# Kernel tuning notes

Hardware: AMD Instinct MI355X
Metric: run time of the kernel (lower is better)

Reference implementation:

```python
import jax, jax.numpy as jnp
import numpy as np

B, N, DIM = 4, 16384, 3
HID = 128            # hidden_dim
CDIM = 128           # feature_dim
RESO = 128           # plane_resolution
R2 = RESO * RESO
NBLK = 5             # n_blocks


def setup_inputs() -> dict:
    key = jax.random.key(0)
    ks = jax.random.split(key, 8)
    s = 0.02
    return {
        "points": jax.random.uniform(ks[0], (B, N, DIM), jnp.float32),  # normalized to [0,1)
        "fc_pos_w": jax.random.normal(ks[1], (2 * HID, DIM), jnp.float32) * s,
        "fc_pos_b": jnp.zeros((2 * HID,), jnp.float32),
        "blk_fc0_w": jax.random.normal(ks[2], (NBLK, HID, 2 * HID), jnp.float32) * s,
        "blk_fc0_b": jnp.zeros((NBLK, HID), jnp.float32),
        "blk_fc1_w": jax.random.normal(ks[3], (NBLK, HID, HID), jnp.float32) * s,
        "blk_fc1_b": jnp.zeros((NBLK, HID), jnp.float32),
        "blk_sc_w": jax.random.normal(ks[4], (NBLK, HID, 2 * HID), jnp.float32) * s,
        "fc_c_w": jax.random.normal(ks[5], (CDIM, HID), jnp.float32) * s,
        "fc_c_b": jnp.zeros((CDIM,), jnp.float32),
    }


def _coord2index(coord_xy):
    # coordinate2index: (coord * reso).long(), then x + reso * y
    g = jnp.clip((coord_xy * RESO).astype(jnp.int32), 0, RESO - 1)  # (B, N, 2)
    return g[..., 0] + RESO * g[..., 1]  # (B, N)


def _resblock(x, w0, b0, w1, b1, ws):
    # ResnetBlockFC: shortcut(x) + fc_1(relu(fc_0(relu(x))))
    h = jax.nn.relu(x) @ w0.T + b0          # (B, N, HID)
    dx = jax.nn.relu(h) @ w1.T + b1         # (B, N, HID)
    return x @ ws.T + dx


def _forward(points, fc_pos_w, fc_pos_b, blk_fc0_w, blk_fc0_b,
             blk_fc1_w, blk_fc1_b, blk_sc_w, fc_c_w, fc_c_b):
    idx = _coord2index(points[..., :2])          # (B, N) int32 plane-bin ids
    net = points @ fc_pos_w.T + fc_pos_b          # (B, N, 2*HID)
    net = _resblock(net, blk_fc0_w[0], blk_fc0_b[0], blk_fc1_w[0], blk_fc1_b[0], blk_sc_w[0])

    seg_max = jax.vmap(lambda f, i: jax.ops.segment_max(f, i, num_segments=R2))
    for k in range(1, NBLK):
        bins = seg_max(net, idx)                                  # (B, R2, HID); empty bins -inf, never gathered
        pooled = jnp.take_along_axis(bins, idx[:, :, None], axis=1)  # (B, N, HID)
        net = _resblock(jnp.concatenate([net, pooled], axis=2),
                        blk_fc0_w[k], blk_fc0_b[k], blk_fc1_w[k], blk_fc1_b[k], blk_sc_w[k])

    net = jax.nn.relu(net) @ fc_c_w.T + fc_c_b    # (B, N, CDIM)

    # generate_plane_features: scatter_mean into zero-initialized plane
    seg_sum = jax.vmap(lambda f, i: jax.ops.segment_sum(f, i, num_segments=R2))
    sums = seg_sum(net, idx)                                      # (B, R2, CDIM)
    cnt = seg_sum(jnp.ones(idx.shape + (1,), net.dtype), idx)     # (B, R2, 1)
    mean = sums / jnp.maximum(cnt, 1.0)                           # empty bins stay 0
    return jnp.transpose(mean, (0, 2, 1)).reshape(B, CDIM, RESO, RESO)


def reference(points, fc_pos_w, fc_pos_b, blk_fc0_w, blk_fc0_b,
              blk_fc1_w, blk_fc1_b, blk_sc_w, fc_c_w, fc_c_b):
    return _forward(points, fc_pos_w, fc_pos_b, blk_fc0_w, blk_fc0_b,
                    blk_fc1_w, blk_fc1_b, blk_sc_w, fc_c_w, fc_c_b)
```

## Files before the change

kernel.cpp:

```cpp
#include <hip/hip_runtime.h>

#define NBATCH 4
#define NPTS   16384
#define BN     (NBATCH * NPTS)

typedef __attribute__((ext_vector_type(8))) _Float16 half8;
typedef __attribute__((ext_vector_type(4))) float f32x4;

#define INV4096 2.44140625e-4f

__device__ __forceinline__ unsigned fenc(float f) {
  unsigned u = __float_as_uint(f);
  return (u & 0x80000000u) ? ~u : (u | 0x80000000u);
}
__device__ __forceinline__ float fdec(unsigned u) {
  unsigned b = (u & 0x80000000u) ? (u & 0x7fffffffu) : ~u;
  return __uint_as_float(b);
}

__device__ __forceinline__ void splith(float x, _Float16& h, _Float16& l) {
  float ax = __builtin_fabsf(x);
  if (ax < 6.1035e-5f) {
    unsigned short sb = (unsigned short)((__float_as_uint(x) >> 16) & 0x8000u);
    h = __builtin_bit_cast(_Float16, sb);
    l = (_Float16)(x * 4096.f);
  } else {
    _Float16 hh = (_Float16)x;
    h = hh;
    l = (_Float16)((x - (float)hh) * 4096.f);
  }
}
__device__ __forceinline__ void splith8(const float v[8], half8& hi, half8& lo) {
  #pragma unroll
  for (int j = 0; j < 8; ++j) { _Float16 h, l; splith(v[j], h, l); hi[j] = h; lo[j] = l; }
}

__device__ __forceinline__ half8 relu8(half8 sgn, half8 v) {
  uint4 s = __builtin_bit_cast(uint4, sgn);
  uint4 x = __builtin_bit_cast(uint4, v);
  unsigned* sp = (unsigned*)&s;
  unsigned* xp = (unsigned*)&x;
  uint4 out;
  unsigned* op = (unsigned*)&out;
  #pragma unroll
  for (int w = 0; w < 4; ++w) {
    unsigned m = sp[w] & 0x80008000u;
    unsigned drop = (m - (m >> 15)) | m;
    op[w] = xp[w] & ~drop;
  }
  return __builtin_bit_cast(half8, out);
}

__global__ void k_zero4(float4* __restrict__ p, int n4) {
  int g = blockIdx.x * 256 + threadIdx.x;
  if (g < n4) p[g] = make_float4(0.f, 0.f, 0.f, 0.f);
}

__global__ void k_idx(const float* __restrict__ pts, int* __restrict__ idx,
                      float* __restrict__ cnt) {
  int g = blockIdx.x * 256 + threadIdx.x;
  if (g >= BN) return;
  int b = g >> 14;
  float px = pts[g * 3 + 0], py = pts[g * 3 + 1];
  int xi = (int)(px * 128.f); xi = xi < 0 ? 0 : (xi > 127 ? 127 : xi);
  int yi = (int)(py * 128.f); yi = yi < 0 ? 0 : (yi > 127 ? 127 : yi);
  int id = xi + (yi << 7);
  idx[g] = id;
  atomicAdd(&cnt[(b << 14) + id], 1.f);
}

__device__ __forceinline__ void pack_slot(const float* __restrict__ src, int K,
                                          _Float16* __restrict__ dhi, int NK,
                                          int slot) {
  int fpt = (K >> 5) << 6;
  int t = slot / fpt, rem = slot - t * fpt;
  int s = rem >> 6, lane = rem & 63;
  int row = (t << 4) + (lane & 15);
  int k0 = (s << 5) + ((lane >> 4) << 3);
  float v[8];
  #pragma unroll
  for (int j = 0; j < 8; ++j) v[j] = src[row * K + k0 + j];
  half8 hi, lo; splith8(v, hi, lo);
  *(half8*)&dhi[(size_t)slot << 3] = hi;
  *(half8*)&dhi[((size_t)slot << 3) + NK] = lo;
}

__global__ void k_pack(const float* __restrict__ fc0w, const float* __restrict__ scw,
                       const float* __restrict__ fc1w, const float* __restrict__ fccw,
                       _Float16* __restrict__ wp) {
  int g = blockIdx.x * 256 + threadIdx.x;
  if (g < 20480) {
    int l = g >> 12, slot = g & 4095;
    pack_slot(fc0w + (size_t)l * 32768, 256, wp + (size_t)l * 65536, 32768, slot);
  } else if (g < 40960) {
    int g2 = g - 20480; int l = g2 >> 12, slot = g2 & 4095;
    pack_slot(scw + (size_t)l * 32768, 256, wp + 327680 + (size_t)l * 65536, 32768, slot);
  } else if (g < 51200) {
    int g2 = g - 40960; int l = g2 >> 11, slot = g2 & 2047;
    pack_slot(fc1w + (size_t)l * 16384, 128, wp + 655360 + (size_t)l * 32768, 16384, slot);
  } else {
    int slot = g - 51200;
    pack_slot(fccw, 128, wp + 819200, 16384, slot);
  }
}

template <int SRC, int POOL>
__launch_bounds__(256, 2)
__global__ void k_rb(const float* __restrict__ pts, const unsigned* __restrict__ binsIn,
                     unsigned* __restrict__ binsOut, const int* __restrict__ idx,
                     const float* __restrict__ posw, const float* __restrict__ posb,
                     const _Float16* __restrict__ w0p, const float* __restrict__ b0,
                     const _Float16* __restrict__ w1p, const float* __restrict__ b1,
                     const _Float16* __restrict__ wsp,
                     float* net) {
  extern __shared__ _Float16 smem[];
  _Float16* Ahi = smem;
  _Float16* Alo = smem + 16384;
  const int tid = threadIdx.x;
  const int lane = tid & 63, wave = tid >> 6;
  const int p0 = blockIdx.x << 6;
  const int b = p0 >> 14;

  #pragma unroll
  for (int i = 0; i < 8; ++i) {
    int sidx = tid + (i << 8);
    int m = sidx >> 5, kslot = sidx & 31, k0 = kslot << 3;
    float v[8];
    if (SRC == 0) {
      const float* pp = &pts[(size_t)(p0 + m) * 3];
      float px = pp[0], py = pp[1], pz = pp[2];
      #pragma unroll
      for (int j = 0; j < 8; ++j) {
        int c = k0 + j;
        v[j] = fmaf(posw[c * 3 + 0], px,
               fmaf(posw[c * 3 + 1], py,
               fmaf(posw[c * 3 + 2], pz, posb[c])));
      }
    } else {
      if (kslot < 16) {
        float4 a = *(const float4*)&net[(size_t)(p0 + m) * 128 + k0];
        float4 c = *(const float4*)&net[(size_t)(p0 + m) * 128 + k0 + 4];
        v[0] = a.x; v[1] = a.y; v[2] = a.z; v[3] = a.w;
        v[4] = c.x; v[5] = c.y; v[6] = c.z; v[7] = c.w;
      } else {
        int rb_ = idx[p0 + m];
        const unsigned* brow = &binsIn[(size_t)(((b << 14) + rb_) << 7) + (k0 - 128)];
        uint4 a = *(const uint4*)brow;
        uint4 c = *(const uint4*)(brow + 4);
        v[0] = fdec(a.x); v[1] = fdec(a.y); v[2] = fdec(a.z); v[3] = fdec(a.w);
        v[4] = fdec(c.x); v[5] = fdec(c.y); v[6] = fdec(c.z); v[7] = fdec(c.w);
      }
    }
    half8 hi, lo; splith8(v, hi, lo);
    int mt = m >> 4, mm = m & 15, s = kslot >> 2, quad = kslot & 3;
    int ln = mm + (quad << 4), kg = (mt << 3) + s;
    int u = (kg << 6) + (ln ^ (kg & 7));
    *(half8*)&Ahi[u << 3] = hi;
    *(half8*)&Alo[u << 3] = lo;
  }
  __syncthreads();

  f32x4 hm[4][2], hc[4][2], so[4][2], sc[4][2];
  {
    int col = lane & 15;
    #pragma unroll
    for (int nt = 0; nt < 2; ++nt) {
      float bv0 = b0[(wave << 5) + (nt << 4) + col];
      float bv1 = b1[(wave << 5) + (nt << 4) + col];
      #pragma unroll
      for (int mt = 0; mt < 4; ++mt) {
        hm[mt][nt] = (f32x4){bv0, bv0, bv0, bv0};
        so[mt][nt] = (f32x4){bv1, bv1, bv1, bv1};
        hc[mt][nt] = (f32x4){0.f, 0.f, 0.f, 0.f};
        sc[mt][nt] = (f32x4){0.f, 0.f, 0.f, 0.f};
      }
    }
  }
  const _Float16* w0lo = w0p + 32768;
  const _Float16* wslo = wsp + 32768;
  for (int ks = 0; ks < 8; ++ks) {
    half8 b0h[2], b0l[2], bsh[2], bsl[2];
    #pragma unroll
    for (int nt = 0; nt < 2; ++nt) {
      int t = (wave << 1) + nt;
      size_t fo = (((size_t)((t << 3) + ks) << 6) + lane) << 3;
      b0h[nt] = *(const half8*)&w0p[fo];
      b0l[nt] = *(const half8*)&w0lo[fo];
      bsh[nt] = *(const half8*)&wsp[fo];
      bsl[nt] = *(const half8*)&wslo[fo];
    }
    #pragma unroll
    for (int mt = 0; mt < 4; ++mt) {
      int kg = (mt << 3) + ks;
      int u = (kg << 6) + (lane ^ (kg & 7));
      half8 ah = *(const half8*)&Ahi[u << 3];
      half8 al = *(const half8*)&Alo[u << 3];
      half8 arh = relu8(ah, ah);
      half8 arl = relu8(ah, al);
      #pragma unroll
      for (int nt = 0; nt < 2; ++nt) {
        hm[mt][nt] = __builtin_amdgcn_mfma_f32_16x16x32_f16(arh, b0h[nt], hm[mt][nt], 0, 0, 0);
        hc[mt][nt] = __builtin_amdgcn_mfma_f32_16x16x32_f16(arl, b0h[nt], hc[mt][nt], 0, 0, 0);
        hc[mt][nt] = __builtin_amdgcn_mfma_f32_16x16x32_f16(arh, b0l[nt], hc[mt][nt], 0, 0, 0);
        so[mt][nt] = __builtin_amdgcn_mfma_f32_16x16x32_f16(ah,  bsh[nt], so[mt][nt], 0, 0, 0);
        sc[mt][nt] = __builtin_amdgcn_mfma_f32_16x16x32_f16(al,  bsh[nt], sc[mt][nt], 0, 0, 0);
        sc[mt][nt] = __builtin_amdgcn_mfma_f32_16x16x32_f16(ah,  bsl[nt], sc[mt][nt], 0, 0, 0);
      }
    }
  }
  __syncthreads();

  _Float16* A2hi = smem;
  _Float16* A2lo = smem + 8192;
  {
    int q = lane >> 4, j2 = lane & 7, qh = (lane & 15) >> 3;
    #pragma unroll
    for (int mt = 0; mt < 4; ++mt) {
      int kg2 = (mt << 2) + wave;
      #pragma unroll
      for (int nt = 0; nt < 2; ++nt) {
        int quad2 = (nt << 1) + qh;
        #pragma unroll
        for (int r = 0; r < 4; ++r) {
          float hv = fmaxf(fmaf(hc[mt][nt][r], INV4096, hm[mt][nt][r]), 0.f);
          _Float16 hb, lb; splith(hv, hb, lb);
          int mm2 = (q << 2) + r;
          int ln2 = mm2 + (quad2 << 4);
          int u2 = (kg2 << 6) + (ln2 ^ (kg2 & 7));
          A2hi[(u2 << 3) + j2] = hb;
          A2lo[(u2 << 3) + j2] = lb;
        }
      }
    }
  }
  __syncthreads();

  const _Float16* w1lo = w1p + 16384;
  for (int ks = 0; ks < 4; ++ks) {
    half8 bh[2], bl[2];
    #pragma unroll
    for (int nt = 0; nt < 2; ++nt) {
      int t = (wave << 1) + nt;
      size_t fo = (((size_t)((t << 2) + ks) << 6) + lane) << 3;
      bh[nt] = *(const half8*)&w1p[fo];
      bl[nt] = *(const half8*)&w1lo[fo];
    }
    #pragma unroll
    for (int mt = 0; mt < 4; ++mt) {
      int kg = (mt << 2) + ks;
      int u = (kg << 6) + (lane ^ (kg & 7));
      half8 ah = *(const half8*)&A2hi[u << 3];
      half8 al = *(const half8*)&A2lo[u << 3];
      #pragma unroll
      for (int nt = 0; nt < 2; ++nt) {
        so[mt][nt] = __builtin_amdgcn_mfma_f32_16x16x32_f16(ah, bh[nt], so[mt][nt], 0, 0, 0);
        sc[mt][nt] = __builtin_amdgcn_mfma_f32_16x16x32_f16(al, bh[nt], sc[mt][nt], 0, 0, 0);
        sc[mt][nt] = __builtin_amdgcn_mfma_f32_16x16x32_f16(ah, bl[nt], sc[mt][nt], 0, 0, 0);
      }
    }
  }

  {
    int col = lane & 15, q = lane >> 4;
    #pragma unroll
    for (int mt = 0; mt < 4; ++mt) {
      #pragma unroll
      for (int r = 0; r < 4; ++r) {
        int m_g = p0 + (mt << 4) + (q << 2) + r;
        int bi = 0;
        if (POOL) bi = ((b << 14) + idx[m_g]) << 7;
        #pragma unroll
        for (int nt = 0; nt < 2; ++nt) {
          int n = (wave << 5) + (nt << 4) + col;
          float v = fmaf(sc[mt][nt][r], INV4096, so[mt][nt][r]);
          net[(size_t)m_g * 128 + n] = v;
          if (POOL) atomicMax(&binsOut[bi + n], fenc(v));
        }
      }
    }
  }
}

__launch_bounds__(256, 2)
__global__ void k_fcc(const float* __restrict__ net, const int* __restrict__ idx,
                      const _Float16* __restrict__ fccp, const float* __restrict__ fccb,
                      float* __restrict__ sums) {
  extern __shared__ _Float16 smem[];
  _Float16* Ahi = smem;
  _Float16* Alo = smem + 8192;
  const int tid = threadIdx.x, lane = tid & 63, wave = tid >> 6;
  const int p0 = blockIdx.x << 6, b = p0 >> 14;
  #pragma unroll
  for (int i = 0; i < 4; ++i) {
    int sidx = tid + (i << 8);
    int m = sidx >> 4, kslot = sidx & 15, k0 = kslot << 3;
    float4 a = *(const float4*)&net[(size_t)(p0 + m) * 128 + k0];
    float4 c = *(const float4*)&net[(size_t)(p0 + m) * 128 + k0 + 4];
    float v[8] = {fmaxf(a.x, 0.f), fmaxf(a.y, 0.f), fmaxf(a.z, 0.f), fmaxf(a.w, 0.f),
                  fmaxf(c.x, 0.f), fmaxf(c.y, 0.f), fmaxf(c.z, 0.f), fmaxf(c.w, 0.f)};
    half8 hi, lo; splith8(v, hi, lo);
    int mt = m >> 4, mm = m & 15, s = kslot >> 2, quad = kslot & 3;
    int ln = mm + (quad << 4), kg = (mt << 2) + s;
    int u = (kg << 6) + (ln ^ (kg & 7));
    *(half8*)&Ahi[u << 3] = hi;
    *(half8*)&Alo[u << 3] = lo;
  }
  __syncthreads();

  f32x4 am[4][2], ac[4][2];
  {
    int col = lane & 15;
    #pragma unroll
    for (int nt = 0; nt < 2; ++nt) {
      float bv = fccb[(wave << 5) + (nt << 4) + col];
      #pragma unroll
      for (int mt = 0; mt < 4; ++mt) {
        am[mt][nt] = (f32x4){bv, bv, bv, bv};
        ac[mt][nt] = (f32x4){0.f, 0.f, 0.f, 0.f};
      }
    }
  }
  const _Float16* flo = fccp + 16384;
  for (int ks = 0; ks < 4; ++ks) {
    half8 bh[2], bl[2];
    #pragma unroll
    for (int nt = 0; nt < 2; ++nt) {
      int t = (wave << 1) + nt;
      size_t fo = (((size_t)((t << 2) + ks) << 6) + lane) << 3;
      bh[nt] = *(const half8*)&fccp[fo];
      bl[nt] = *(const half8*)&flo[fo];
    }
    #pragma unroll
    for (int mt = 0; mt < 4; ++mt) {
      int kg = (mt << 2) + ks;
      int u = (kg << 6) + (lane ^ (kg & 7));
      half8 ah = *(const half8*)&Ahi[u << 3];
      half8 al = *(const half8*)&Alo[u << 3];
      #pragma unroll
      for (int nt = 0; nt < 2; ++nt) {
        am[mt][nt] = __builtin_amdgcn_mfma_f32_16x16x32_f16(ah, bh[nt], am[mt][nt], 0, 0, 0);
        ac[mt][nt] = __builtin_amdgcn_mfma_f32_16x16x32_f16(al, bh[nt], ac[mt][nt], 0, 0, 0);
        ac[mt][nt] = __builtin_amdgcn_mfma_f32_16x16x32_f16(ah, bl[nt], ac[mt][nt], 0, 0, 0);
      }
    }
  }
  {
    int col = lane & 15, q = lane >> 4;
    #pragma unroll
    for (int mt = 0; mt < 4; ++mt) {
      #pragma unroll
      for (int r = 0; r < 4; ++r) {
        int m_g = p0 + (mt << 4) + (q << 2) + r;
        int bi = ((b << 14) + idx[m_g]) << 7;
        #pragma unroll
        for (int nt = 0; nt < 2; ++nt) {
          int n = (wave << 5) + (nt << 4) + col;
          atomicAdd(&sums[bi + n], fmaf(ac[mt][nt][r], INV4096, am[mt][nt][r]));
        }
      }
    }
  }
}

__launch_bounds__(256)
__global__ void k_finalize(const float* __restrict__ sums, const float* __restrict__ cnt,
                           float* __restrict__ out) {
  __shared__ float t[64 * 65];
  __shared__ float rc[64];
  const int bid = blockIdx.x;
  const int ct = bid & 1, rt = (bid >> 1) & 255, b = bid >> 9;
  const int r0 = rt << 6, c0 = ct << 6;
  const int tid = threadIdx.x, l16 = tid & 15, sl = tid >> 4;
  for (int rr = sl; rr < 64; rr += 16) {
    float4 v = *(const float4*)&sums[(size_t)((b << 14) + r0 + rr) * 128 + c0 + (l16 << 2)];
    int cb = l16 << 2;
    t[rr * 65 + cb + 0] = v.x; t[rr * 65 + cb + 1] = v.y;
    t[rr * 65 + cb + 2] = v.z; t[rr * 65 + cb + 3] = v.w;
  }
  if (tid < 64) rc[tid] = 1.f / fmaxf(cnt[(b << 14) + r0 + tid], 1.f);
  __syncthreads();
  for (int cc = sl; cc < 64; cc += 16) {
    int c = c0 + cc;
    int rb = l16 << 2;
    float4 o = make_float4(t[(rb + 0) * 65 + cc] * rc[rb + 0],
                           t[(rb + 1) * 65 + cc] * rc[rb + 1],
                           t[(rb + 2) * 65 + cc] * rc[rb + 2],
                           t[(rb + 3) * 65 + cc] * rc[rb + 3]);
    *(float4*)&out[(size_t)((b << 7) + c) * 16384 + r0 + rb] = o;
  }
}

extern "C" void kernel_launch(void* const* d_in, const int* in_sizes, int n_in,
                              void* d_out, int out_size, void* d_ws, size_t ws_size,
                              hipStream_t stream) {
  const float* points = (const float*)d_in[0];
  const float* posw   = (const float*)d_in[1];
  const float* posb   = (const float*)d_in[2];
  const float* fc0w   = (const float*)d_in[3];
  const float* fc0b   = (const float*)d_in[4];
  const float* fc1w   = (const float*)d_in[5];
  const float* fc1b   = (const float*)d_in[6];
  const float* scw    = (const float*)d_in[7];
  const float* fccw   = (const float*)d_in[8];
  const float* fccb   = (const float*)d_in[9];
  float* outp = (float*)d_out;

  float* net = (float*)d_ws;
  unsigned* bins0 = (unsigned*)(net + (size_t)BN * 128);
  unsigned* bins1 = bins0 + (size_t)8388608;
  int* idxp = (int*)(bins1 + (size_t)8388608);
  float* cnt = (float*)(idxp + BN);
  _Float16* wp = (_Float16*)(cnt + 65536);

  const _Float16* w0_ = wp;
  const _Float16* ws_ = wp + 327680;
  const _Float16* w1_ = wp + 655360;
  const _Float16* fcc_ = wp + 819200;

  k_zero4<<<64, 256, 0, stream>>>((float4*)cnt, 16384);
  k_idx<<<256, 256, 0, stream>>>(points, idxp, cnt);
  k_pack<<<208, 256, 0, stream>>>(fc0w, scw, fc1w, fccw, wp);

  k_zero4<<<8192, 256, 0, stream>>>((float4*)bins0, 2097152);
  k_rb<0, 1><<<1024, 256, 65536, stream>>>(points, nullptr, bins0, idxp, posw, posb,
                                           w0_, fc0b, w1_, fc1b, ws_, net);
  unsigned* bin_in = bins0;
  unsigned* bin_out = bins1;
  for (int l = 1; l < 4; ++l) {
    k_zero4<<<8192, 256, 0, stream>>>((float4*)bin_out, 2097152);
    k_rb<1, 1><<<1024, 256, 65536, stream>>>(points, bin_in, bin_out, idxp, posw, posb,
                                             w0_ + (size_t)l * 65536, fc0b + l * 128,
                                             w1_ + (size_t)l * 32768, fc1b + l * 128,
                                             ws_ + (size_t)l * 65536, net);
    unsigned* tsw = bin_in; bin_in = bin_out; bin_out = tsw;
  }
  k_zero4<<<8192, 256, 0, stream>>>((float4*)bin_out, 2097152);
  k_rb<1, 0><<<1024, 256, 65536, stream>>>(points, bin_in, nullptr, idxp, posw, posb,
                                           w0_ + (size_t)4 * 65536, fc0b + 4 * 128,
                                           w1_ + (size_t)4 * 32768, fc1b + 4 * 128,
                                           ws_ + (size_t)4 * 65536, net);
  float* sums = (float*)bin_out;
  k_fcc<<<1024, 256, 32768, stream>>>(net, idxp, fcc_, fccb, sums);
  k_finalize<<<2048, 256, 0, stream>>>(sums, cnt, outp);
}
```

Measured before the change: 455.4 us.

## Halve point tile per block and double-buffer weight fragments in MFMA loops

Shrinks the rows per block from 64 to 32 points in the resblock and fc_c kernels, halving LDS and accumulator registers. The grid doubles and launch bounds rise to four blocks per SIMD-group so more waves can hide latency. It also software-pipelines the weight fragment loads, fetching the next k-step's B fragments while the current MFMAs run. In exchange each weight fragment is reused across only two row tiles instead of four, so global and L2 weight traffic per point doubles. The prefetch also adds live registers and wastes one extra load on the final iteration.

```diff
diff --git a/kernel.cpp b/kernel.cpp
--- a/kernel.cpp
+++ b/kernel.cpp
@@ -105,7 +105,7 @@
 }
 
 template <int SRC, int POOL>
-__launch_bounds__(256, 2)
+__launch_bounds__(256, 4)
 __global__ void k_rb(const float* __restrict__ pts, const unsigned* __restrict__ binsIn,
                      unsigned* __restrict__ binsOut, const int* __restrict__ idx,
                      const float* __restrict__ posw, const float* __restrict__ posb,
@@ -115,14 +115,14 @@
                      float* net) {
   extern __shared__ _Float16 smem[];
   _Float16* Ahi = smem;
-  _Float16* Alo = smem + 16384;
+  _Float16* Alo = smem + 8192;
   const int tid = threadIdx.x;
   const int lane = tid & 63, wave = tid >> 6;
-  const int p0 = blockIdx.x << 6;
+  const int p0 = blockIdx.x << 5;
   const int b = p0 >> 14;
 
   #pragma unroll
-  for (int i = 0; i < 8; ++i) {
+  for (int i = 0; i < 4; ++i) {
     int sidx = tid + (i << 8);
     int m = sidx >> 5, kslot = sidx & 31, k0 = kslot << 3;
     float v[8];
@@ -160,7 +160,7 @@
   }
   __syncthreads();
 
-  f32x4 hm[4][2], hc[4][2], so[4][2], sc[4][2];
+  f32x4 hm[2][2], hc[2][2], so[2][2], sc[2][2];
   {
     int col = lane & 15;
     #pragma unroll
@@ -168,7 +168,7 @@
       float bv0 = b0[(wave << 5) + (nt << 4) + col];
       float bv1 = b1[(wave << 5) + (nt << 4) + col];
       #pragma unroll
-      for (int mt = 0; mt < 4; ++mt) {
+      for (int mt = 0; mt < 2; ++mt) {
         hm[mt][nt] = (f32x4){bv0, bv0, bv0, bv0};
         so[mt][nt] = (f32x4){bv1, bv1, bv1, bv1};
         hc[mt][nt] = (f32x4){0.f, 0.f, 0.f, 0.f};
@@ -178,19 +178,31 @@
   }
   const _Float16* w0lo = w0p + 32768;
   const _Float16* wslo = wsp + 32768;
+
+  half8 c0h[2], c0l[2], csh[2], csl[2];
+  #pragma unroll
+  for (int nt = 0; nt < 2; ++nt) {
+    int t = (wave << 1) + nt;
+    size_t fo = (((size_t)(t << 3) << 6) + lane) << 3;
+    c0h[nt] = *(const half8*)&w0p[fo];
+    c0l[nt] = *(const half8*)&w0lo[fo];
+    csh[nt] = *(const half8*)&wsp[fo];
+    csl[nt] = *(const half8*)&wslo[fo];
+  }
   for (int ks = 0; ks < 8; ++ks) {
-    half8 b0h[2], b0l[2], bsh[2], bsl[2];
+    half8 n0h[2], n0l[2], nsh[2], nsl[2];
+    int ksn = (ks + 1) & 7;
     #pragma unroll
     for (int nt = 0; nt < 2; ++nt) {
       int t = (wave << 1) + nt;
-      size_t fo = (((size_t)((t << 3) + ks) << 6) + lane) << 3;
-      b0h[nt] = *(const half8*)&w0p[fo];
-      b0l[nt] = *(const half8*)&w0lo[fo];
-      bsh[nt] = *(const half8*)&wsp[fo];
-      bsl[nt] = *(const half8*)&wslo[fo];
-    }
-    #pragma unroll
-    for (int mt = 0; mt < 4; ++mt) {
+      size_t fo = (((size_t)((t << 3) + ksn) << 6) + lane) << 3;
+      n0h[nt] = *(const half8*)&w0p[fo];
+      n0l[nt] = *(const half8*)&w0lo[fo];
+      nsh[nt] = *(const half8*)&wsp[fo];
+      nsl[nt] = *(const half8*)&wslo[fo];
+    }
+    #pragma unroll
+    for (int mt = 0; mt < 2; ++mt) {
       int kg = (mt << 3) + ks;
       int u = (kg << 6) + (lane ^ (kg & 7));
       half8 ah = *(const half8*)&Ahi[u << 3];
@@ -199,23 +211,28 @@
       half8 arl = relu8(ah, al);
       #pragma unroll
       for (int nt = 0; nt < 2; ++nt) {
-        hm[mt][nt] = __builtin_amdgcn_mfma_f32_16x16x32_f16(arh, b0h[nt], hm[mt][nt], 0, 0, 0);
-        hc[mt][nt] = __builtin_amdgcn_mfma_f32_16x16x32_f16(arl, b0h[nt], hc[mt][nt], 0, 0, 0);
-        hc[mt][nt] = __builtin_amdgcn_mfma_f32_16x16x32_f16(arh, b0l[nt], hc[mt][nt], 0, 0, 0);
-        so[mt][nt] = __builtin_amdgcn_mfma_f32_16x16x32_f16(ah,  bsh[nt], so[mt][nt], 0, 0, 0);
-        sc[mt][nt] = __builtin_amdgcn_mfma_f32_16x16x32_f16(al,  bsh[nt], sc[mt][nt], 0, 0, 0);
-        sc[mt][nt] = __builtin_amdgcn_mfma_f32_16x16x32_f16(ah,  bsl[nt], sc[mt][nt], 0, 0, 0);
-      }
+        hm[mt][nt] = __builtin_amdgcn_mfma_f32_16x16x32_f16(arh, c0h[nt], hm[mt][nt], 0, 0, 0);
+        hc[mt][nt] = __builtin_amdgcn_mfma_f32_16x16x32_f16(arl, c0h[nt], hc[mt][nt], 0, 0, 0);
+        hc[mt][nt] = __builtin_amdgcn_mfma_f32_16x16x32_f16(arh, c0l[nt], hc[mt][nt], 0, 0, 0);
+        so[mt][nt] = __builtin_amdgcn_mfma_f32_16x16x32_f16(ah,  csh[nt], so[mt][nt], 0, 0, 0);
+        sc[mt][nt] = __builtin_amdgcn_mfma_f32_16x16x32_f16(al,  csh[nt], sc[mt][nt], 0, 0, 0);
+        sc[mt][nt] = __builtin_amdgcn_mfma_f32_16x16x32_f16(ah,  csl[nt], sc[mt][nt], 0, 0, 0);
+      }
+    }
+    #pragma unroll
+    for (int nt = 0; nt < 2; ++nt) {
+      c0h[nt] = n0h[nt]; c0l[nt] = n0l[nt];
+      csh[nt] = nsh[nt]; csl[nt] = nsl[nt];
     }
   }
   __syncthreads();
 
   _Float16* A2hi = smem;
-  _Float16* A2lo = smem + 8192;
+  _Float16* A2lo = smem + 4096;
   {
     int q = lane >> 4, j2 = lane & 7, qh = (lane & 15) >> 3;
     #pragma unroll
-    for (int mt = 0; mt < 4; ++mt) {
+    for (int mt = 0; mt < 2; ++mt) {
       int kg2 = (mt << 2) + wave;
       #pragma unroll
       for (int nt = 0; nt < 2; ++nt) {
@@ -236,34 +253,45 @@
   __syncthreads();
 
   const _Float16* w1lo = w1p + 16384;
+  half8 w1ch[2], w1cl[2];
+  #pragma unroll
+  for (int nt = 0; nt < 2; ++nt) {
+    int t = (wave << 1) + nt;
+    size_t fo = (((size_t)(t << 2) << 6) + lane) << 3;
+    w1ch[nt] = *(const half8*)&w1p[fo];
+    w1cl[nt] = *(const half8*)&w1lo[fo];
+  }
   for (int ks = 0; ks < 4; ++ks) {
-    half8 bh[2], bl[2];
+    half8 nh[2], nl[2];
+    int ksn = (ks + 1) & 3;
     #pragma unroll
     for (int nt = 0; nt < 2; ++nt) {
       int t = (wave << 1) + nt;
-      size_t fo = (((size_t)((t << 2) + ks) << 6) + lane) << 3;
-      bh[nt] = *(const half8*)&w1p[fo];
-      bl[nt] = *(const half8*)&w1lo[fo];
-    }
-    #pragma unroll
-    for (int mt = 0; mt < 4; ++mt) {
+      size_t fo = (((size_t)((t << 2) + ksn) << 6) + lane) << 3;
+      nh[nt] = *(const half8*)&w1p[fo];
+      nl[nt] = *(const half8*)&w1lo[fo];
+    }
+    #pragma unroll
+    for (int mt = 0; mt < 2; ++mt) {
       int kg = (mt << 2) + ks;
       int u = (kg << 6) + (lane ^ (kg & 7));
       half8 ah = *(const half8*)&A2hi[u << 3];
       half8 al = *(const half8*)&A2lo[u << 3];
       #pragma unroll
       for (int nt = 0; nt < 2; ++nt) {
-        so[mt][nt] = __builtin_amdgcn_mfma_f32_16x16x32_f16(ah, bh[nt], so[mt][nt], 0, 0, 0);
-        sc[mt][nt] = __builtin_amdgcn_mfma_f32_16x16x32_f16(al, bh[nt], sc[mt][nt], 0, 0, 0);
-        sc[mt][nt] = __builtin_amdgcn_mfma_f32_16x16x32_f16(ah, bl[nt], sc[mt][nt], 0, 0, 0);
-      }
-    }
+        so[mt][nt] = __builtin_amdgcn_mfma_f32_16x16x32_f16(ah, w1ch[nt], so[mt][nt], 0, 0, 0);
+        sc[mt][nt] = __builtin_amdgcn_mfma_f32_16x16x32_f16(al, w1ch[nt], sc[mt][nt], 0, 0, 0);
+        sc[mt][nt] = __builtin_amdgcn_mfma_f32_16x16x32_f16(ah, w1cl[nt], sc[mt][nt], 0, 0, 0);
+      }
+    }
+    #pragma unroll
+    for (int nt = 0; nt < 2; ++nt) { w1ch[nt] = nh[nt]; w1cl[nt] = nl[nt]; }
   }
 
   {
     int col = lane & 15, q = lane >> 4;
     #pragma unroll
-    for (int mt = 0; mt < 4; ++mt) {
+    for (int mt = 0; mt < 2; ++mt) {
       #pragma unroll
       for (int r = 0; r < 4; ++r) {
         int m_g = p0 + (mt << 4) + (q << 2) + r;
@@ -281,17 +309,17 @@
   }
 }
 
-__launch_bounds__(256, 2)
+__launch_bounds__(256, 4)
 __global__ void k_fcc(const float* __restrict__ net, const int* __restrict__ idx,
                       const _Float16* __restrict__ fccp, const float* __restrict__ fccb,
                       float* __restrict__ sums) {
   extern __shared__ _Float16 smem[];
   _Float16* Ahi = smem;
-  _Float16* Alo = smem + 8192;
+  _Float16* Alo = smem + 4096;
   const int tid = threadIdx.x, lane = tid & 63, wave = tid >> 6;
-  const int p0 = blockIdx.x << 6, b = p0 >> 14;
-  #pragma unroll
-  for (int i = 0; i < 4; ++i) {
+  const int p0 = blockIdx.x << 5, b = p0 >> 14;
+  #pragma unroll
+  for (int i = 0; i < 2; ++i) {
     int sidx = tid + (i << 8);
     int m = sidx >> 4, kslot = sidx & 15, k0 = kslot << 3;
     float4 a = *(const float4*)&net[(size_t)(p0 + m) * 128 + k0];
@@ -307,47 +335,58 @@
   }
   __syncthreads();
 
-  f32x4 am[4][2], ac[4][2];
+  f32x4 am[2][2], ac[2][2];
   {
     int col = lane & 15;
     #pragma unroll
     for (int nt = 0; nt < 2; ++nt) {
       float bv = fccb[(wave << 5) + (nt << 4) + col];
       #pragma unroll
-      for (int mt = 0; mt < 4; ++mt) {
+      for (int mt = 0; mt < 2; ++mt) {
         am[mt][nt] = (f32x4){bv, bv, bv, bv};
         ac[mt][nt] = (f32x4){0.f, 0.f, 0.f, 0.f};
       }
     }
   }
   const _Float16* flo = fccp + 16384;
+  half8 ch[2], cl[2];
+  #pragma unroll
+  for (int nt = 0; nt < 2; ++nt) {
+    int t = (wave << 1) + nt;
+    size_t fo = (((size_t)(t << 2) << 6) + lane) << 3;
+    ch[nt] = *(const half8*)&fccp[fo];
+    cl[nt] = *(const half8*)&flo[fo];
+  }
   for (int ks = 0; ks < 4; ++ks) {
-    half8 bh[2], bl[2];
+    half8 nh[2], nl[2];
+    int ksn = (ks + 1) & 3;
     #pragma unroll
     for (int nt = 0; nt < 2; ++nt) {
       int t = (wave << 1) + nt;
-      size_t fo = (((size_t)((t << 2) + ks) << 6) + lane) << 3;
-      bh[nt] = *(const half8*)&fccp[fo];
-      bl[nt] = *(const half8*)&flo[fo];
-    }
-    #pragma unroll
-    for (int mt = 0; mt < 4; ++mt) {
+      size_t fo = (((size_t)((t << 2) + ksn) << 6) + lane) << 3;
+      nh[nt] = *(const half8*)&fccp[fo];
+      nl[nt] = *(const half8*)&flo[fo];
+    }
+    #pragma unroll
+    for (int mt = 0; mt < 2; ++mt) {
       int kg = (mt << 2) + ks;
       int u = (kg << 6) + (lane ^ (kg & 7));
       half8 ah = *(const half8*)&Ahi[u << 3];
       half8 al = *(const half8*)&Alo[u << 3];
       #pragma unroll
       for (int nt = 0; nt < 2; ++nt) {
-        am[mt][nt] = __builtin_amdgcn_mfma_f32_16x16x32_f16(ah, bh[nt], am[mt][nt], 0, 0, 0);
-        ac[mt][nt] = __builtin_amdgcn_mfma_f32_16x16x32_f16(al, bh[nt], ac[mt][nt], 0, 0, 0);
-        ac[mt][nt] = __builtin_amdgcn_mfma_f32_16x16x32_f16(ah, bl[nt], ac[mt][nt], 0, 0, 0);
-      }
-    }
+        am[mt][nt] = __builtin_amdgcn_mfma_f32_16x16x32_f16(ah, ch[nt], am[mt][nt], 0, 0, 0);
+        ac[mt][nt] = __builtin_amdgcn_mfma_f32_16x16x32_f16(al, ch[nt], ac[mt][nt], 0, 0, 0);
+        ac[mt][nt] = __builtin_amdgcn_mfma_f32_16x16x32_f16(ah, cl[nt], ac[mt][nt], 0, 0, 0);
+      }
+    }
+    #pragma unroll
+    for (int nt = 0; nt < 2; ++nt) { ch[nt] = nh[nt]; cl[nt] = nl[nt]; }
   }
   {
     int col = lane & 15, q = lane >> 4;
     #pragma unroll
-    for (int mt = 0; mt < 4; ++mt) {
+    for (int mt = 0; mt < 2; ++mt) {
       #pragma unroll
       for (int r = 0; r < 4; ++r) {
         int m_g = p0 + (mt << 4) + (q << 2) + r;
@@ -422,24 +461,24 @@
   k_pack<<<208, 256, 0, stream>>>(fc0w, scw, fc1w, fccw, wp);
 
   k_zero4<<<8192, 256, 0, stream>>>((float4*)bins0, 2097152);
-  k_rb<0, 1><<<1024, 256, 65536, stream>>>(points, nullptr, bins0, idxp, posw, posb,
+  k_rb<0, 1><<<2048, 256, 32768, stream>>>(points, nullptr, bins0, idxp, posw, posb,
                                            w0_, fc0b, w1_, fc1b, ws_, net);
   unsigned* bin_in = bins0;
   unsigned* bin_out = bins1;
   for (int l = 1; l < 4; ++l) {
     k_zero4<<<8192, 256, 0, stream>>>((float4*)bin_out, 2097152);
-    k_rb<1, 1><<<1024, 256, 65536, stream>>>(points, bin_in, bin_out, idxp, posw, posb,
+    k_rb<1, 1><<<2048, 256, 32768, stream>>>(points, bin_in, bin_out, idxp, posw, posb,
                                              w0_ + (size_t)l * 65536, fc0b + l * 128,
                                              w1_ + (size_t)l * 32768, fc1b + l * 128,
                                              ws_ + (size_t)l * 65536, net);
     unsigned* tsw = bin_in; bin_in = bin_out; bin_out = tsw;
   }
   k_zero4<<<8192, 256, 0, stream>>>((float4*)bin_out, 2097152);
-  k_rb<1, 0><<<1024, 256, 65536, stream>>>(points, bin_in, nullptr, idxp, posw, posb,
+  k_rb<1, 0><<<2048, 256, 32768, stream>>>(points, bin_in, nullptr, idxp, posw, posb,
                                            w0_ + (size_t)4 * 65536, fc0b + 4 * 128,
                                            w1_ + (size_t)4 * 32768, fc1b + 4 * 128,
                                            ws_ + (size_t)4 * 65536, net);
   float* sums = (float*)bin_out;
-  k_fcc<<<1024, 256, 32768, stream>>>(net, idxp, fcc_, fccb, sums);
+  k_fcc<<<2048, 256, 16384, stream>>>(net, idxp, fcc_, fccb, sums);
   k_finalize<<<2048, 256, 0, stream>>>(sums, cnt, outp);
 }
```

After: 466.5 us. 1.02x slower.
